# Kernel tuning notes

Hardware: AMD Instinct MI355X
Metric: run time of the kernel (lower is better)

Reference implementation:

```python
import jax, jax.numpy as jnp
import numpy as np

N_NODES = 51200      # 128 graphs * 400 ROIs
N_ROI = 400
HID = 64             # 'batch_size' arg of the torch module = hidden channels = n_timepoints
N_EDGES = 1638400    # avg degree 32
N_CLASSES = 2
NEG_SLOPE = 0.01


def setup_inputs():
    key = jax.random.key(0)
    ks = jax.random.split(key, 20)
    s = 0.05
    inp = {
        'x': jax.random.normal(ks[0], (N_NODES, HID), dtype=jnp.float32),
        'edge_index': jax.random.randint(ks[1], (2, N_EDGES), 0, N_NODES, dtype=jnp.int64),
        'edge_weight': jax.random.uniform(ks[2], (N_EDGES,), dtype=jnp.float32),
        # GCNConv weights stored [in, out]; biases [out]
        'W1': jax.random.normal(ks[3], (HID, HID), dtype=jnp.float32) * s,
        'b1': jnp.zeros((HID,), jnp.float32),
        'W2': jax.random.normal(ks[4], (HID, HID), dtype=jnp.float32) * s,
        'b2': jnp.zeros((HID,), jnp.float32),
        'W3': jax.random.normal(ks[5], (HID, HID), dtype=jnp.float32) * s,
        'b3': jnp.zeros((HID,), jnp.float32),
        'W4': jax.random.normal(ks[6], (HID, HID), dtype=jnp.float32) * s,
        'b4': jnp.zeros((HID,), jnp.float32),
        'fc1_w': jax.random.normal(ks[7], (N_ROI * HID, 256), dtype=jnp.float32) * 0.01,
        'fc1_b': jnp.zeros((256,), jnp.float32),
        'fc2_w': jax.random.normal(ks[8], (256, 128), dtype=jnp.float32) * s,
        'fc2_b': jnp.zeros((128,), jnp.float32),
        'fc3_w': jax.random.normal(ks[9], (128, N_CLASSES), dtype=jnp.float32) * s,
        'fc3_b': jnp.zeros((N_CLASSES,), jnp.float32),
    }
    return inp


def _gcn_norm(edge_index, edge_weight, n):
    # PyG GCNConv: add self-loops (weight 1), symmetric D^-1/2 A D^-1/2 normalization
    loop = jnp.arange(n, dtype=edge_index.dtype)
    src = jnp.concatenate([edge_index[0], loop])
    dst = jnp.concatenate([edge_index[1], loop])
    w = jnp.concatenate([edge_weight, jnp.ones((n,), edge_weight.dtype)])
    deg = jax.ops.segment_sum(w, dst, num_segments=n)
    dis = jnp.where(deg > 0, jax.lax.rsqrt(jnp.maximum(deg, 1e-30)), 0.0)
    norm = dis[src] * w * dis[dst]
    return src, dst, norm


def _conv(h, W, b, src, dst, norm, n):
    h = h @ W                                   # [N, out]
    msg = h[src] * norm[:, None]                # gather + scale
    out = jax.ops.segment_sum(msg, dst, num_segments=n) + b
    return out


def _leaky(v):
    return jnp.where(v >= 0, v, NEG_SLOPE * v)


def _head(h, fc1_w, fc1_b, fc2_w, fc2_b, fc3_w, fc3_b):
    # global_mean_pool with batch = arange(N) is identity; pool == reshape to graphs
    g = h.reshape(-1, N_ROI * HID)              # [G, n_roi*hid]
    g = g @ fc1_w + fc1_b                       # dropout is eval-mode identity
    g = g @ fc2_w + fc2_b
    g = g @ fc3_w + fc3_b
    return g


def reference(x, edge_index, edge_weight, W1, b1, W2, b2, W3, b3, W4, b4,
              fc1_w, fc1_b, fc2_w, fc2_b, fc3_w, fc3_b):
    n = x.shape[0]
    src, dst, norm = _gcn_norm(edge_index, edge_weight, n)
    h = _leaky(_conv(x, W1, b1, src, dst, norm, n))
    h = _leaky(_conv(h, W2, b2, src, dst, norm, n))
    h = _leaky(_conv(h, W3, b3, src, dst, norm, n))
    h = _leaky(_conv(h, W4, b4, src, dst, norm, n))
    logits = _head(h, fc1_w, fc1_b, fc2_w, fc2_b, fc3_w, fc3_b)
    logits0 = _head(x, fc1_w, fc1_b, fc2_w, fc2_b, fc3_w, fc3_b)
    penal = 0.09 * logits.shape[0] / jnp.linalg.norm(logits - logits0)
    return logits, penal
```

## Files before the change

kernel.cpp:

```cpp
#include <hip/hip_runtime.h>
#include <cstddef>

#define N_NODES 51200
#define N_EDGES 1638400
#define HID 64
#define N_ROI 400
#define N_GRAPHS 128
#define KHEAD 25600
#define NEG_SLOPE 0.01f
#define CAP 80
#define NCHUNK 400
#define CHUNK 4096
#define NBIN 512
#define BINSZ 100
#define LSTRIDE 81

typedef unsigned short u16;
typedef unsigned int u32;
typedef unsigned char u8;
typedef float f32x2 __attribute__((ext_vector_type(2)));

__device__ inline u16 f2bf(float f) {
    u32 u = __float_as_uint(f);
    u32 r = u + 0x7FFFu + ((u >> 16) & 1u);
    return (u16)(r >> 16);
}
__device__ inline float bf2f(u16 h) { return __uint_as_float(((u32)h) << 16); }

__device__ inline f32x2 dec8lo(u32 v) { return __builtin_amdgcn_cvt_pk_f32_fp8((int)v, false); }
__device__ inline f32x2 dec8hi(u32 v) { return __builtin_amdgcn_cvt_pk_f32_fp8((int)v, true); }
template <bool HI>
__device__ inline u32 enc8(float a, float b, u32 old) {
    return (u32)__builtin_amdgcn_cvt_pk_fp8_f32(a, b, (int)old, HI);
}
__device__ inline u32 pack4_fp8(float a, float b, float c, float d) {
    u32 w = enc8<false>(a, b, 0u);
    return enc8<true>(c, d, w);
}


__global__ __launch_bounds__(1024) void k1(const int* __restrict__ ei,
                                           const float* __restrict__ ew,
                                           uint2* __restrict__ chunkData,
                                           u32* __restrict__ offcnt,
                                           const float* __restrict__ x,
                                           u8* __restrict__ x8,
                                           const float* __restrict__ fc2w,
                                           const float* __restrict__ fc3w,
                                           const float* __restrict__ fc1b,
                                           const float* __restrict__ fc2b,
                                           const float* __restrict__ fc3b,
                                           float* __restrict__ fc23,
                                           float* __restrict__ bc) {
    int bid = blockIdx.x, t = threadIdx.x;
    __shared__ u32 cnt[NBIN];
    __shared__ u32 scan[NBIN];
    __shared__ u32 cur[NBIN];
    __shared__ uint2 stag[CHUNK];
    __shared__ float t1[128];

    if (bid < NCHUNK) {
        if (t < NBIN) cnt[t] = 0;
        __syncthreads();
        int base = bid * CHUNK;
        u32 lo[4]; float wv[4]; int bin[4];
        #pragma unroll
        for (int i = 0; i < 4; i++) {
            int e = base + i * 1024 + t;
            int s = ei[e], d = ei[N_EDGES + e];
            wv[i] = ew[e];
            bin[i] = d / BINSZ;
            lo[i] = (u32)s | ((u32)(d - bin[i] * BINSZ) << 16);
            atomicAdd(&cnt[bin[i]], 1u);
        }
        __syncthreads();
        if (t < NBIN) scan[t] = cnt[t];
        __syncthreads();
        for (int off = 1; off < NBIN; off <<= 1) {
            u32 add = (t < NBIN && t >= off) ? scan[t - off] : 0u;
            __syncthreads();
            if (t < NBIN) scan[t] += add;
            __syncthreads();
        }
        if (t < NBIN) cur[t] = scan[t] - cnt[t];
        __syncthreads();
        if (t < NBIN) offcnt[(size_t)bid * NBIN + t] = cur[t] | (cnt[t] << 16);
        __syncthreads();
        #pragma unroll
        for (int i = 0; i < 4; i++) {
            u32 pos = atomicAdd(&cur[bin[i]], 1u);
            stag[pos] = make_uint2(lo[i], __float_as_uint(wv[i]));
        }
        __syncthreads();
        #pragma unroll
        for (int i = 0; i < 4; i++)
            chunkData[base + i * 1024 + t] = stag[i * 1024 + t];
    } else if (bid < 600) {
        int idx = (bid - NCHUNK) * 1024 + t;
        const float4* xp = reinterpret_cast<const float4*>(x) + (size_t)idx * 4;
        float4 a = xp[0], b = xp[1], c = xp[2], d = xp[3];
        reinterpret_cast<uint4*>(x8)[idx] =
            make_uint4(pack4_fp8(a.x, a.y, a.z, a.w), pack4_fp8(b.x, b.y, b.z, b.w),
                       pack4_fp8(c.x, c.y, c.z, c.w), pack4_fp8(d.x, d.y, d.z, d.w));
    } else {
        if (t < 256) {
            float s0 = 0.f, s1 = 0.f;
            const float* row = fc2w + t * 128;
            for (int j = 0; j < 128; j++) {
                float a = row[j];
                s0 += a * fc3w[2 * j];
                s1 += a * fc3w[2 * j + 1];
            }
            fc23[2 * t] = s0;
            fc23[2 * t + 1] = s1;
        }
        if (t < 128) {
            float s = fc2b[t];
            for (int k = 0; k < 256; k++) s += fc1b[k] * fc2w[k * 128 + t];
            t1[t] = s;
        }
        __syncthreads();
        if (t < 2) {
            float s = fc3b[t];
            for (int j = 0; j < 128; j++) s += t1[j] * fc3w[2 * j + t];
            bc[t] = s;
        }
    }
}


__global__ __launch_bounds__(256) void k1t(const u32* __restrict__ in,
                                           u32* __restrict__ outT) {
    __shared__ u32 tile[32][33];
    int cx = blockIdx.x % 13, by = blockIdx.x / 13;
    int c0 = cx * 32, b0 = by * 32;
    int tx = threadIdx.x & 31, ty = threadIdx.x >> 5;
    for (int i = ty; i < 32; i += 8) {
        int c = c0 + i;
        if (c < NCHUNK) tile[i][tx] = in[(size_t)c * NBIN + b0 + tx];
    }
    __syncthreads();
    for (int i = ty; i < 32; i += 8) {
        int b = b0 + i;
        int c = c0 + tx;
        if (c < NCHUNK) outT[(size_t)b * NCHUNK + c] = tile[tx][i];
    }
}


__global__ __launch_bounds__(512) void k2(const uint2* __restrict__ chunkData,
                                          const u32* __restrict__ offcntT,
                                          u32* __restrict__ buck,
                                          int* __restrict__ cnts,
                                          float* __restrict__ dis,
                                          const float* __restrict__ fc1w,
                                          const float* __restrict__ fc23,
                                          float* __restrict__ Wc) {
    int bid = blockIdx.x, t = threadIdx.x;
    __shared__ u32 lbuck[BINSZ * LSTRIDE];
    __shared__ u32 lcnt[BINSZ];
    __shared__ float ldeg[BINSZ];
    __shared__ u32 oc[NCHUNK];

    if (bid < NBIN) {
        if (t < BINSZ) { lcnt[t] = 0; ldeg[t] = 0.f; }
        if (t < NCHUNK) oc[t] = offcntT[(size_t)bid * NCHUNK + t];
        __syncthreads();
        int w = t >> 6, lane = t & 63;
        int sBase = w * 50;
        for (int j = 0; j < 56; j += 8) {
            int s = sBase + j + (lane >> 3);
            int i0 = lane & 7;
            int k = 0, off = 0;
            if (j + (lane >> 3) < 50) {
                u32 o = oc[s];
                off = (int)(o & 0xffffu);
                k = (int)(o >> 16);
            }
            const uint2* cd = chunkData + (size_t)s * CHUNK + off;
            for (int i = i0; i < k; i += 8) {
                uint2 e = cd[i];
                u32 node = e.x >> 16;
                u32 src = e.x & 0xffffu;
                float ww = __uint_as_float(e.y);
                u32 pos = atomicAdd(&lcnt[node], 1u);
                if (pos < CAP - 1) lbuck[node * LSTRIDE + pos] = ((u32)f2bf(ww) << 16) | src;
                atomicAdd(&ldeg[node], ww);
            }
        }
        __syncthreads();
        int sg = t >> 5, ln = t & 31;
        for (int n = sg; n < BINSZ; n += 16) {
            int node = bid * BINSZ + n;
            int k = min((int)lcnt[n], CAP - 1);
            u32* dst = buck + (size_t)node * CAP;
            for (int i = ln; i < k; i += 32) dst[i] = lbuck[n * LSTRIDE + i];
            if (ln == 0) {
                cnts[node] = k;
                dis[node] = rsqrtf(1.f + ldeg[n]);
            }
        }
    } else {
        float* f23 = (float*)lbuck;
        f23[t] = fc23[t];
        __syncthreads();
        int r = (bid - NBIN) * 512 + t;
        const float* row = fc1w + (size_t)r * 256;
        float s0 = 0.f, s1 = 0.f;
        #pragma unroll 8
        for (int k = 0; k < 256; k++) {
            float a = row[k];
            s0 += a * f23[2 * k];
            s1 += a * f23[2 * k + 1];
        }
        Wc[2 * r] = s0;
        Wc[2 * r + 1] = s1;
    }
}


__global__ __launch_bounds__(1024) void k3(u32* __restrict__ buck,
                                           int* __restrict__ cnts,
                                           const float* __restrict__ dis) {
    int gt = blockIdx.x * 1024 + threadIdx.x;
    int node = gt >> 5, sub = gt & 31;
    float d = dis[node];
    int k = cnts[node];
    u32* bk = buck + (size_t)node * CAP;
    for (int j = sub; j < k; j += 32) {
        u32 e = bk[j];
        float val = bf2f((u16)(e >> 16)) * d * dis[e & 0xffffu];
        bk[j] = ((u32)f2bf(val) << 16) | (e & 0xffffu);
    }
    if (sub == 0) {
        bk[k] = ((u32)f2bf(d * d) << 16) | (u32)node;
        cnts[node] = k + 1;
    }
}


__global__ __launch_bounds__(512) void k_layer(const u8* __restrict__ H8,
                                               const u32* __restrict__ buck,
                                               const int* __restrict__ cnts,
                                               const float* __restrict__ W,
                                               const float* __restrict__ bias,
                                               u8* __restrict__ Hout) {
    __shared__ float Ws[64][64];
    __shared__ float ZsT[64][33];
    int t = threadIdx.x;
    int base = blockIdx.x * 32;

    #pragma unroll
    for (int i = 0; i < 2; i++) {
        int f = t + i * 512;
        int kk = f >> 4, c4 = f & 15;
        float4 wv = reinterpret_cast<const float4*>(W)[f];
        *reinterpret_cast<float4*>(&Ws[kk][c4 * 4]) = wv;
    }

    int grp = t >> 4, sub = t & 15;
    int node = base + grp;
    int k = cnts[node];
    const u32* bk = buck + (size_t)node * CAP;
    const u8* Hb = H8 + sub * 4;
    float a0 = 0.f, a1 = 0.f, a2 = 0.f, a3 = 0.f;
    for (int j0 = 0; j0 < k; j0 += 16) {
        int idx = j0 + sub;
        u32 pre = (idx < k) ? bk[idx] : 0u;
        #pragma unroll
        for (int i = 0; i < 16; i++) {
            u32 e = (u32)__shfl((int)pre, i, 16);
            float val = __uint_as_float(e & 0xffff0000u);
            u32 src = e & 0xffffu;
            u32 r = *reinterpret_cast<const u32*>(Hb + (size_t)src * HID);
            f32x2 lo = dec8lo(r), hi = dec8hi(r);
            a0 += val * lo.x; a1 += val * lo.y;
            a2 += val * hi.x; a3 += val * hi.y;
        }
    }
    ZsT[4 * sub + 0][grp] = a0;
    ZsT[4 * sub + 1][grp] = a1;
    ZsT[4 * sub + 2][grp] = a2;
    ZsT[4 * sub + 3][grp] = a3;
    __syncthreads();

    int r = t >> 4, c4 = t & 15;
    float4 acc = {0.f, 0.f, 0.f, 0.f};
    #pragma unroll 8
    for (int kk = 0; kk < 64; kk++) {
        float a = ZsT[kk][r];
        const float4 w = *reinterpret_cast<const float4*>(&Ws[kk][c4 * 4]);
        acc.x += a * w.x; acc.y += a * w.y; acc.z += a * w.z; acc.w += a * w.w;
    }
    float4 bb = reinterpret_cast<const float4*>(bias)[c4];
    float v0 = acc.x + bb.x, v1 = acc.y + bb.y, v2 = acc.z + bb.z, v3 = acc.w + bb.w;
    v0 = v0 >= 0.f ? v0 : NEG_SLOPE * v0;
    v1 = v1 >= 0.f ? v1 : NEG_SLOPE * v1;
    v2 = v2 >= 0.f ? v2 : NEG_SLOPE * v2;
    v3 = v3 >= 0.f ? v3 : NEG_SLOPE * v3;
    *reinterpret_cast<u32*>(Hout + (size_t)(base + r) * HID + c4 * 4) =
        pack4_fp8(v0, v1, v2, v3);
}


__global__ __launch_bounds__(256) void k_logits(const u8* __restrict__ h4,
                                                const float* __restrict__ x,
                                                const float* __restrict__ Wc,
                                                const float* __restrict__ bc,
                                                float* __restrict__ out,
                                                float* __restrict__ sq,
                                                int* __restrict__ done) {
    int g = blockIdx.x, t = threadIdx.x;
    const u8* bh = h4 + (size_t)g * KHEAD;
    const float* bx = x + (size_t)g * KHEAD;
    float aH0 = 0.f, aH1 = 0.f, aX0 = 0.f, aX1 = 0.f;
    for (int k2 = t; k2 < KHEAD / 2; k2 += 256) {
        u32 hv = reinterpret_cast<const u16*>(bh)[k2];
        f32x2 h = dec8lo(hv);
        float2 xv = reinterpret_cast<const float2*>(bx)[k2];
        float4 wc = reinterpret_cast<const float4*>(Wc)[k2];
        aH0 += h.x * wc.x + h.y * wc.z;
        aH1 += h.x * wc.y + h.y * wc.w;
        aX0 += xv.x * wc.x + xv.y * wc.z;
        aX1 += xv.x * wc.y + xv.y * wc.w;
    }
    for (int off = 32; off > 0; off >>= 1) {
        aH0 += __shfl_down(aH0, off);
        aH1 += __shfl_down(aH1, off);
        aX0 += __shfl_down(aX0, off);
        aX1 += __shfl_down(aX1, off);
    }
    __shared__ float red[4][4];
    int wave = t >> 6, lane = t & 63;
    if (lane == 0) {
        red[wave][0] = aH0; red[wave][1] = aH1;
        red[wave][2] = aX0; red[wave][3] = aX1;
    }
    __syncthreads();
    if (t == 0) {
        float h0 = red[0][0] + red[1][0] + red[2][0] + red[3][0];
        float h1 = red[0][1] + red[1][1] + red[2][1] + red[3][1];
        float x0 = red[0][2] + red[1][2] + red[2][2] + red[3][2];
        float x1 = red[0][3] + red[1][3] + red[2][3] + red[3][3];
        out[2 * g]     = h0 + bc[0];
        out[2 * g + 1] = h1 + bc[1];
        float d0 = h0 - x0, d1 = h1 - x1;
        atomicAdd(sq, d0 * d0 + d1 * d1);
        __threadfence();
        int c = atomicAdd(done, 1);
        if (c == N_GRAPHS - 1) {
            __threadfence();
            float s = atomicAdd(sq, 0.f);
            out[2 * N_GRAPHS] = 0.09f * (float)N_GRAPHS / sqrtf(s);
        }
    }
}


extern "C" void kernel_launch(void* const* d_in, const int* in_sizes, int n_in,
                              void* d_out, int out_size, void* d_ws, size_t ws_size,
                              hipStream_t stream) {
    const float* x    = (const float*)d_in[0];
    const int*   ei   = (const int*)d_in[1];
    const float* ew   = (const float*)d_in[2];
    const float* W1   = (const float*)d_in[3];
    const float* b1   = (const float*)d_in[4];
    const float* W2   = (const float*)d_in[5];
    const float* b2   = (const float*)d_in[6];
    const float* W3   = (const float*)d_in[7];
    const float* b3   = (const float*)d_in[8];
    const float* W4   = (const float*)d_in[9];
    const float* b4   = (const float*)d_in[10];
    const float* fc1w = (const float*)d_in[11];
    const float* fc1b = (const float*)d_in[12];
    const float* fc2w = (const float*)d_in[13];
    const float* fc2b = (const float*)d_in[14];
    const float* fc3w = (const float*)d_in[15];
    const float* fc3b = (const float*)d_in[16];
    float* out = (float*)d_out;

    char* base = (char*)d_ws;
    size_t off = 0;
    auto alloc = [&](size_t bytes) -> void* {
        void* p = base + off;
        off += (bytes + 255) & ~(size_t)255;
        return p;
    };
    uint2* chunkData = (uint2*)alloc((size_t)N_EDGES * 8);
    u32*   offcnt    = (u32*)alloc((size_t)NCHUNK * NBIN * 4);
    u32*   offcntT   = (u32*)alloc((size_t)NCHUNK * NBIN * 4);
    u32*   buck      = (u32*)alloc((size_t)N_NODES * CAP * 4);
    int*   cnts      = (int*)alloc((size_t)N_NODES * 4);
    float* dis       = (float*)alloc((size_t)N_NODES * 4);
    u8*    x8        = (u8*)alloc((size_t)N_NODES * HID);
    u8*    ha        = (u8*)alloc((size_t)N_NODES * HID);
    u8*    hb        = (u8*)alloc((size_t)N_NODES * HID);
    float* fc23      = (float*)alloc(512 * 4);
    float* bc        = (float*)alloc(2 * 4);
    float* Wc        = (float*)alloc((size_t)KHEAD * 2 * 4);
    char*  ctrl      = (char*)alloc(256);
    float* sq        = (float*)ctrl;
    int*   done      = (int*)(ctrl + 4);

    (void)hipMemsetAsync(ctrl, 0, 8, stream);
    k1<<<601, 1024, 0, stream>>>(ei, ew, chunkData, offcnt, x, x8,
                                 fc2w, fc3w, fc1b, fc2b, fc3b, fc23, bc);
    k1t<<<13 * 16, 256, 0, stream>>>(offcnt, offcntT);
    k2<<<NBIN + 50, 512, 0, stream>>>(chunkData, offcntT, buck, cnts, dis,
                                      fc1w, fc23, Wc);
    k3<<<1600, 1024, 0, stream>>>(buck, cnts, dis);

    const float* Wl[4] = {W1, W2, W3, W4};
    const float* bl[4] = {b1, b2, b3, b4};
    u8* hbufs[2] = {ha, hb};
    const u8* hin = x8;
    for (int l = 0; l < 4; l++) {
        u8* hout = hbufs[l & 1];
        k_layer<<<N_NODES / 32, 512, 0, stream>>>(hin, buck, cnts,
                                                  Wl[l], bl[l], hout);
        hin = hout;
    }

    k_logits<<<N_GRAPHS, 256, 0, stream>>>(hin, x, Wc, bc, out, sq, done);
}
```

Baseline: 192.1 us.

## Rebalance edge binning into larger chunks and finer bins with a wave-shuffle scan

The edge-sorting preprocessing now uses 200 chunks of 8192 edges and 1024 destination bins of 50 nodes, replacing 400 chunks and 512 bins. In k1 each thread loads edges with vectorized int4/float4 reads and computes the bin prefix sum with a wave-level shuffle scan plus a small cross-wave pass, replacing the multi-barrier block scan. The k1t transpose and k2 gather loops are resized to the new geometry, and k_layer indexes the fp8 feature rows as 32-bit words. The aim is to cut barrier and launch overhead in the binning stages and give k2 more, smaller bins to parallelize over, at the cost of more per-chunk work and a different load balance.

```diff
diff --git a/kernel.cpp b/kernel.cpp
--- a/kernel.cpp
+++ b/kernel.cpp
@@ -9,10 +9,10 @@
 #define KHEAD 25600
 #define NEG_SLOPE 0.01f
 #define CAP 80
-#define NCHUNK 400
-#define CHUNK 4096
-#define NBIN 512
-#define BINSZ 100
+#define NCHUNK 200
+#define CHUNK 8192
+#define NBIN 1024
+#define BINSZ 50
 #define LSTRIDE 81
 
 typedef unsigned short u16;
@@ -54,48 +54,63 @@
                                            float* __restrict__ bc) {
     int bid = blockIdx.x, t = threadIdx.x;
     __shared__ u32 cnt[NBIN];
-    __shared__ u32 scan[NBIN];
     __shared__ u32 cur[NBIN];
+    __shared__ u32 wsum[16];
     __shared__ uint2 stag[CHUNK];
     __shared__ float t1[128];
 
     if (bid < NCHUNK) {
-        if (t < NBIN) cnt[t] = 0;
+        cnt[t] = 0;
         __syncthreads();
         int base = bid * CHUNK;
-        u32 lo[4]; float wv[4]; int bin[4];
+        const int4* sp = reinterpret_cast<const int4*>(ei + base);
+        const int4* dp = reinterpret_cast<const int4*>(ei + N_EDGES + base);
+        const float4* wp = reinterpret_cast<const float4*>(ew + base);
+        int4 sa = sp[2 * t], sb = sp[2 * t + 1];
+        int4 da = dp[2 * t], db = dp[2 * t + 1];
+        float4 wa = wp[2 * t], wb = wp[2 * t + 1];
+        int ss[8] = {sa.x, sa.y, sa.z, sa.w, sb.x, sb.y, sb.z, sb.w};
+        int dd[8] = {da.x, da.y, da.z, da.w, db.x, db.y, db.z, db.w};
+        float wv[8] = {wa.x, wa.y, wa.z, wa.w, wb.x, wb.y, wb.z, wb.w};
+        u32 lo[8]; int bin[8];
         #pragma unroll
-        for (int i = 0; i < 4; i++) {
-            int e = base + i * 1024 + t;
-            int s = ei[e], d = ei[N_EDGES + e];
-            wv[i] = ew[e];
-            bin[i] = d / BINSZ;
-            lo[i] = (u32)s | ((u32)(d - bin[i] * BINSZ) << 16);
-            atomicAdd(&cnt[bin[i]], 1u);
-        }
-        __syncthreads();
-        if (t < NBIN) scan[t] = cnt[t];
-        __syncthreads();
-        for (int off = 1; off < NBIN; off <<= 1) {
-            u32 add = (t < NBIN && t >= off) ? scan[t - off] : 0u;
-            __syncthreads();
-            if (t < NBIN) scan[t] += add;
-            __syncthreads();
-        }
-        if (t < NBIN) cur[t] = scan[t] - cnt[t];
-        __syncthreads();
-        if (t < NBIN) offcnt[(size_t)bid * NBIN + t] = cur[t] | (cnt[t] << 16);
-        __syncthreads();
+        for (int i = 0; i < 8; i++) {
+            int b = (int)((u32)dd[i] / BINSZ);
+            bin[i] = b;
+            lo[i] = (u32)ss[i] | ((u32)(dd[i] - b * BINSZ) << 16);
+            atomicAdd(&cnt[b], 1u);
+        }
+        __syncthreads();
+        int wave = t >> 6, lane = t & 63;
+        u32 v = cnt[t], inc = v;
         #pragma unroll
-        for (int i = 0; i < 4; i++) {
+        for (int d = 1; d < 64; d <<= 1) {
+            u32 o = __shfl_up(inc, d, 64);
+            if (lane >= d) inc += o;
+        }
+        if (lane == 63) wsum[wave] = inc;
+        __syncthreads();
+        if (t == 0) {
+            u32 r = 0;
+            #pragma unroll
+            for (int i = 0; i < 16; i++) { u32 c = wsum[i]; wsum[i] = r; r += c; }
+        }
+        __syncthreads();
+        u32 excl = inc - v + wsum[wave];
+        cur[t] = excl;
+        offcnt[(size_t)bid * NBIN + t] = excl | (v << 16);
+        __syncthreads();
+        #pragma unroll
+        for (int i = 0; i < 8; i++) {
             u32 pos = atomicAdd(&cur[bin[i]], 1u);
             stag[pos] = make_uint2(lo[i], __float_as_uint(wv[i]));
         }
         __syncthreads();
+        const uint4* sg4 = reinterpret_cast<const uint4*>(stag);
+        uint4* out4 = reinterpret_cast<uint4*>(chunkData + (size_t)base);
         #pragma unroll
-        for (int i = 0; i < 4; i++)
-            chunkData[base + i * 1024 + t] = stag[i * 1024 + t];
-    } else if (bid < 600) {
+        for (int i = 0; i < 4; i++) out4[i * 1024 + t] = sg4[i * 1024 + t];
+    } else if (bid < 400) {
         int idx = (bid - NCHUNK) * 1024 + t;
         const float4* xp = reinterpret_cast<const float4*>(x) + (size_t)idx * 4;
         float4 a = xp[0], b = xp[1], c = xp[2], d = xp[3];
@@ -132,8 +147,8 @@
 __global__ __launch_bounds__(256) void k1t(const u32* __restrict__ in,
                                            u32* __restrict__ outT) {
     __shared__ u32 tile[32][33];
-    int cx = blockIdx.x % 13, by = blockIdx.x / 13;
-    int c0 = cx * 32, b0 = by * 32;
+    int bx = blockIdx.x & 31, cy = blockIdx.x >> 5;
+    int b0 = bx * 32, c0 = cy * 32;
     int tx = threadIdx.x & 31, ty = threadIdx.x >> 5;
     for (int i = ty; i < 32; i += 8) {
         int c = c0 + i;
@@ -167,12 +182,13 @@
         if (t < NCHUNK) oc[t] = offcntT[(size_t)bid * NCHUNK + t];
         __syncthreads();
         int w = t >> 6, lane = t & 63;
-        int sBase = w * 50;
-        for (int j = 0; j < 56; j += 8) {
-            int s = sBase + j + (lane >> 3);
+        int sBase = w * 25;
+        for (int j = 0; j < 32; j += 8) {
+            int so = j + (lane >> 3);
+            int s = sBase + so;
             int i0 = lane & 7;
             int k = 0, off = 0;
-            if (j + (lane >> 3) < 50) {
+            if (so < 25) {
                 u32 o = oc[s];
                 off = (int)(o & 0xffffu);
                 k = (int)(o >> 16);
@@ -262,7 +278,7 @@
     int node = base + grp;
     int k = cnts[node];
     const u32* bk = buck + (size_t)node * CAP;
-    const u8* Hb = H8 + sub * 4;
+    const u32* H32 = reinterpret_cast<const u32*>(H8);
     float a0 = 0.f, a1 = 0.f, a2 = 0.f, a3 = 0.f;
     for (int j0 = 0; j0 < k; j0 += 16) {
         int idx = j0 + sub;
@@ -272,7 +288,7 @@
             u32 e = (u32)__shfl((int)pre, i, 16);
             float val = __uint_as_float(e & 0xffff0000u);
             u32 src = e & 0xffffu;
-            u32 r = *reinterpret_cast<const u32*>(Hb + (size_t)src * HID);
+            u32 r = H32[src * 16 + sub];
             f32x2 lo = dec8lo(r), hi = dec8hi(r);
             a0 += val * lo.x; a1 += val * lo.y;
             a2 += val * hi.x; a3 += val * hi.y;
@@ -403,9 +419,9 @@
     int*   done      = (int*)(ctrl + 4);
 
     (void)hipMemsetAsync(ctrl, 0, 8, stream);
-    k1<<<601, 1024, 0, stream>>>(ei, ew, chunkData, offcnt, x, x8,
+    k1<<<401, 1024, 0, stream>>>(ei, ew, chunkData, offcnt, x, x8,
                                  fc2w, fc3w, fc1b, fc2b, fc3b, fc23, bc);
-    k1t<<<13 * 16, 256, 0, stream>>>(offcnt, offcntT);
+    k1t<<<224, 256, 0, stream>>>(offcnt, offcntT);
     k2<<<NBIN + 50, 512, 0, stream>>>(chunkData, offcntT, buck, cnts, dis,
                                       fc1w, fc23, Wc);
     k3<<<1600, 1024, 0, stream>>>(buck, cnts, dis);
```

Result: no change. 192.8 us (+0.4%).
